# Optimization experiments

Hardware: AMD Instinct MI355X
Metric: run time of the kernel (lower is better)

Reference implementation:

```python
import jax, jax.numpy as jnp
import numpy as np

N_NODES = 100000
N_EDGES = 1600000
NUM_GRAPHS = 1000

def gcn_conv(x, edge_index, W, b, n):
    # PyG GCNConv: out = D^-1/2 (A + I) D^-1/2 (x W) + b
    xw = x @ W                                   # [n, F_out]
    loop = jnp.arange(n, dtype=edge_index.dtype)
    src = jnp.concatenate([edge_index[0], loop])  # sources (messages come from src)
    dst = jnp.concatenate([edge_index[1], loop])  # targets (aggregated into dst)
    deg = jnp.zeros((n,), xw.dtype).at[dst].add(1.0)
    dinv = jnp.where(deg > 0, jax.lax.rsqrt(deg), 0.0)
    norm = dinv[src] * dinv[dst]                  # [E+n]
    msg = xw[src] * norm[:, None]                 # gather + scale
    out = jax.ops.segment_sum(msg, dst, num_segments=n)
    return out + b

def scatter_mean(x, seg, num_segments):
    sums = jax.ops.segment_sum(x, seg, num_segments=num_segments)
    cnt = jax.ops.segment_sum(jnp.ones((x.shape[0],), x.dtype), seg, num_segments=num_segments)
    return sums / jnp.maximum(cnt, 1.0)[:, None]

def setup_inputs() -> dict:
    key = jax.random.key(0)
    ks = jax.random.split(key, 9)
    x = jax.random.normal(ks[0], (N_NODES, 256), dtype=jnp.float32)
    edge_index = jax.random.randint(ks[1], (2, N_EDGES), 0, N_NODES, dtype=jnp.int64 if jax.config.jax_enable_x64 else jnp.int32).astype(jnp.int32)
    batch = jnp.sort(jax.random.randint(ks[2], (N_NODES,), 0, NUM_GRAPHS)).astype(jnp.int32)
    W1 = jax.random.normal(ks[3], (256, 128), dtype=jnp.float32) * 0.05
    b1 = jax.random.normal(ks[4], (128,), dtype=jnp.float32) * 0.05
    W2 = jax.random.normal(ks[5], (128, 64), dtype=jnp.float32) * 0.05
    b2 = jax.random.normal(ks[6], (64,), dtype=jnp.float32) * 0.05
    fc_W = jax.random.normal(ks[7], (64, 4), dtype=jnp.float32) * 0.05
    fc_b = jax.random.normal(ks[8], (4,), dtype=jnp.float32) * 0.05
    return {"x": x, "edge_index": edge_index, "batch": batch, "W1": W1, "b1": b1, "W2": W2, "b2": b2, "fc_W": fc_W, "fc_b": fc_b}

def reference(x, edge_index, batch, W1, b1, W2, b2, fc_W, fc_b):
    n = x.shape[0]
    h = gcn_conv(x, edge_index, W1, b1, n)
    h = jax.nn.relu(h)                 # dropout p=0.0 is identity
    h = gcn_conv(h, edge_index, W2, b2, n)
    g = scatter_mean(h, batch, NUM_GRAPHS)   # [G, out_feats]
    logits = g @ fc_W + fc_b
    return jax.nn.log_softmax(logits, axis=1)
```

## Files before the change

### kernel.cpp

```cpp
#include <hip/hip_runtime.h>
#include <hip/hip_bf16.h>

#define N_NODES 100000
#define N_EDGES 1600000
#define NUM_GRAPHS 1000

#define NODES_PER_BUCKET 256
#define BUCKET_SHIFT 8
#define NBUCKETS 391
#define CAP 5120

#define G1_BLOCKS 1563
#define FUSED_BLOCKS 2345
#define FILL_CHUNK 2052

typedef __attribute__((ext_vector_type(8))) short short8;
typedef __attribute__((ext_vector_type(4))) float f32x4;
typedef __attribute__((ext_vector_type(2))) float f32x2;
typedef unsigned short ushort;

__device__ __forceinline__ ushort f2bf(float f) {
    unsigned int u = __float_as_uint(f);
    u = u + 0x7fffu + ((u >> 16) & 1u);
    return (ushort)(u >> 16);
}
__device__ __forceinline__ float bflo(unsigned int u) { return __uint_as_float(u << 16); }
__device__ __forceinline__ float bfhi(unsigned int u) { return __uint_as_float(u & 0xffff0000u); }

__device__ __forceinline__ unsigned char f2fp8(float f) {
    return (unsigned char)(__builtin_amdgcn_cvt_pk_fp8_f32(f, f, 0, false) & 0xff);
}

__global__ void setup_kernel(int* __restrict__ bcursor,
                             const float* __restrict__ W1, ushort* __restrict__ W1t,
                             const float* __restrict__ W2, ushort* __restrict__ W2t,
                             float* __restrict__ gsum, float* __restrict__ gcnt) {
    int b = blockIdx.x, tid = threadIdx.x;
    if (b < 2) {
        int i = b * 256 + tid;
        if (i < NBUCKETS) bcursor[i] = i * CAP;
    } else if (b < 130) {
        int idx = (b - 2) * 256 + tid;
        int n = idx & 127, k = idx >> 7;
        W1t[n * 256 + k] = f2bf(W1[k * 128 + n]);
    } else if (b < 162) {
        int idx = (b - 130) * 256 + tid;
        int n = idx & 63, k = idx >> 6;
        W2t[n * 128 + k] = f2bf(W2[k * 64 + n]);
    } else {
        int idx = (b - 162) * 256 + tid;
        if (idx < NUM_GRAPHS * 64) gsum[idx] = 0.f;
        else if (idx < NUM_GRAPHS * 64 + NUM_GRAPHS) gcnt[idx - NUM_GRAPHS * 64] = 0.f;
    }
}
#define SETUP_BLOCKS 416

__global__ __launch_bounds__(256) void gemm1_fill_kernel(const float* __restrict__ x,
                                                         const ushort* __restrict__ W1t,
                                                         unsigned char* __restrict__ outb,
                                                         const int* __restrict__ esrc,
                                                         const int* __restrict__ edst,
                                                         int* __restrict__ bcursor,
                                                         int* __restrict__ pairs) {
    __shared__ ushort Ab[64 * 32];
    __shared__ ushort Bb[128 * 32];
    const int b = blockIdx.x;
    const int tid = threadIdx.x;

    if (b % 3 == 2) {
        int* scnt = (int*)Ab;
        int* spos = (int*)Bb;
        const int fid = b / 3;
        const int beg = fid * FILL_CHUNK;
        int end = beg + FILL_CHUNK;
        if (end > N_EDGES) end = N_EDGES;
        if (beg >= end) return;
        for (int i = tid; i < NBUCKETS; i += 256) scnt[i] = 0;
        __syncthreads();
        for (int e = beg + tid * 4; e < end; e += 1024) {
            int4 d4 = *(const int4*)&edst[e];
            atomicAdd(&scnt[d4.x >> BUCKET_SHIFT], 1);
            atomicAdd(&scnt[d4.y >> BUCKET_SHIFT], 1);
            atomicAdd(&scnt[d4.z >> BUCKET_SHIFT], 1);
            atomicAdd(&scnt[d4.w >> BUCKET_SHIFT], 1);
        }
        __syncthreads();
        for (int i = tid; i < NBUCKETS; i += 256) {
            int c = scnt[i];
            spos[i] = c > 0 ? atomicAdd(&bcursor[i], c) : 0;
        }
        __syncthreads();
        for (int e = beg + tid * 4; e < end; e += 1024) {
            int4 d4 = *(const int4*)&edst[e];
            int4 s4 = *(const int4*)&esrc[e];
            int p0 = atomicAdd(&spos[d4.x >> BUCKET_SHIFT], 1);
            pairs[p0] = (s4.x << 8) | (d4.x & 255);
            int p1 = atomicAdd(&spos[d4.y >> BUCKET_SHIFT], 1);
            pairs[p1] = (s4.y << 8) | (d4.y & 255);
            int p2 = atomicAdd(&spos[d4.z >> BUCKET_SHIFT], 1);
            pairs[p2] = (s4.z << 8) | (d4.z & 255);
            int p3 = atomicAdd(&spos[d4.w >> BUCKET_SHIFT], 1);
            pairs[p3] = (s4.w << 8) | (d4.w & 255);
        }
        return;
    }

    const int gid = b - (b + 1) / 3;
    if (gid >= G1_BLOCKS) return;
    const int row0 = gid * 64;
    const int wv = tid >> 6;
    const int l = tid & 63;
    const int lrow = l & 15;
    const int quad = l >> 4;

    const int ar = tid >> 2;
    const int ak = (tid & 3) * 8;
    int grow = row0 + ar;
    if (grow > N_NODES - 1) grow = N_NODES - 1;
    const float* xrow = x + (size_t)grow * 256;
    const int bn = tid >> 1;
    const int bk = (tid & 1) * 16;

    f32x4 acc[8];
#pragma unroll
    for (int t = 0; t < 8; ++t) acc[t] = (f32x4){0.f, 0.f, 0.f, 0.f};

    for (int kc = 0; kc < 8; ++kc) {
        float4 a0 = *(const float4*)&xrow[kc * 32 + ak];
        float4 a1 = *(const float4*)&xrow[kc * 32 + ak + 4];
        const ushort* wt = &W1t[(size_t)bn * 256 + kc * 32 + bk];
        uint4 w0 = *(const uint4*)wt;
        uint4 w1 = *(const uint4*)(wt + 8);

        if (kc > 0) __syncthreads();
        ushort av[8];
        av[0] = f2bf(a0.x); av[1] = f2bf(a0.y); av[2] = f2bf(a0.z); av[3] = f2bf(a0.w);
        av[4] = f2bf(a1.x); av[5] = f2bf(a1.y); av[6] = f2bf(a1.z); av[7] = f2bf(a1.w);
        *(uint4*)&Ab[ar * 32 + ak] = *(uint4*)av;
        *(uint4*)&Bb[bn * 32 + bk] = w0;
        *(uint4*)&Bb[bn * 32 + bk + 8] = w1;
        __syncthreads();

        short8 afrag = *(const short8*)&Ab[(wv * 16 + lrow) * 32 + quad * 8];
#pragma unroll
        for (int t = 0; t < 8; ++t) {
            short8 bfrag = *(const short8*)&Bb[(t * 16 + lrow) * 32 + quad * 8];
            acc[t] = __builtin_amdgcn_mfma_f32_16x16x32_bf16(afrag, bfrag, acc[t], 0, 0, 0);
        }
    }

    const int rbase = row0 + wv * 16 + quad * 4;
#pragma unroll
    for (int t = 0; t < 8; ++t) {
#pragma unroll
        for (int r = 0; r < 4; ++r) {
            int row = rbase + r;
            if (row < N_NODES)
                outb[(size_t)row * 128 + t * 16 + lrow] = f2fp8(acc[t][r]);
        }
    }
}

__global__ __launch_bounds__(256) void csr_fill_local_kernel(const int* __restrict__ pairs,
                                                             const int* __restrict__ bcursor,
                                                             int* __restrict__ csr_src,
                                                             int* __restrict__ row_beg,
                                                             int* __restrict__ row_end,
                                                             float* __restrict__ dinv) {
    __shared__ int plds[CAP];
    __shared__ int hist[256];
    __shared__ int scanv[256];
    __shared__ int cur[256];
    const int b = blockIdx.x;
    const int base = b * CAP;
    const int tid = threadIdx.x;
    const int cnt_b = bcursor[b] - base;

    for (int i = tid; i < cnt_b; i += 256) plds[i] = pairs[base + i];
    hist[tid] = 0;
    __syncthreads();
    for (int i = tid; i < cnt_b; i += 256) atomicAdd(&hist[plds[i] & 255], 1);
    __syncthreads();

    int deg = hist[tid];
    scanv[tid] = deg;
    for (int off = 1; off < 256; off <<= 1) {
        __syncthreads();
        int add = (tid >= off) ? scanv[tid - off] : 0;
        __syncthreads();
        scanv[tid] += add;
    }
    __syncthreads();
    int excl = scanv[tid] - deg;

    int node = b * NODES_PER_BUCKET + tid;
    if (node < N_NODES) {
        int beg = base + excl;
        row_beg[node] = beg;
        row_end[node] = beg + deg;
        dinv[node] = rsqrtf((float)(deg + 1));
    }
    cur[tid] = excl;
    __syncthreads();

    for (int i = tid; i < cnt_b; i += 256) {
        int pr = plds[i];
        int pos = base + atomicAdd(&cur[pr & 255], 1);
        csr_src[pos] = ((unsigned int)pr) >> 8;
    }
}

__global__ __launch_bounds__(256) void agg1_kernel(const unsigned int* __restrict__ xw,
                                                   const int* __restrict__ csr_src,
                                                   const int* __restrict__ row_beg,
                                                   const int* __restrict__ row_end,
                                                   const float* __restrict__ dinv,
                                                   const float* __restrict__ bias,
                                                   ushort* __restrict__ h) {
    const int wave = threadIdx.x >> 6;
    const int lane = threadIdx.x & 63;
    const int h2 = lane >> 5;
    const int c = lane & 31;
    const int node = blockIdx.x * 8 + wave * 2 + h2;

    const int beg = row_beg[node], end = row_end[node];
    const float dvn = rsqrtf((float)(end - beg + 1));

    unsigned int sv = xw[(size_t)node * 32 + c];
    f32x2 slo = __builtin_amdgcn_cvt_pk_f32_fp8(sv, false);
    f32x2 shi = __builtin_amdgcn_cvt_pk_f32_fp8(sv, true);
    float a0 = dvn * slo[0], a1 = dvn * slo[1], a2 = dvn * shi[0], a3 = dvn * shi[1];

    for (int e = beg; e < end; e += 16) {
        int s[16];
        s[0] = csr_src[e];
#pragma unroll
        for (int i = 1; i < 16; ++i)
            s[i] = (e + i < end) ? csr_src[e + i] : s[0];
        unsigned int v[16];
        float ds[16];
#pragma unroll
        for (int i = 0; i < 16; ++i) {
            v[i] = xw[(size_t)s[i] * 32 + c];
            ds[i] = dinv[s[i]];
        }
#pragma unroll
        for (int i = 0; i < 16; ++i) {
            if (i == 0 || e + i < end) {
                f32x2 lo = __builtin_amdgcn_cvt_pk_f32_fp8(v[i], false);
                f32x2 hi = __builtin_amdgcn_cvt_pk_f32_fp8(v[i], true);
                a0 += ds[i] * lo[0]; a1 += ds[i] * lo[1];
                a2 += ds[i] * hi[0]; a3 += ds[i] * hi[1];
            }
        }
    }
    float4 bv = *(const float4*)&bias[c * 4];
    float v0 = a0 * dvn + bv.x, v1 = a1 * dvn + bv.y;
    float v2 = a2 * dvn + bv.z, v3 = a3 * dvn + bv.w;
    ushort4 o;
    o.x = f2bf(v0 > 0.f ? v0 : 0.f);
    o.y = f2bf(v1 > 0.f ? v1 : 0.f);
    o.z = f2bf(v2 > 0.f ? v2 : 0.f);
    o.w = f2bf(v3 > 0.f ? v3 : 0.f);
    *(ushort4*)&h[(size_t)node * 128 + c * 4] = o;
}

__global__ __launch_bounds__(256) void gemm2_kernel(const ushort* __restrict__ h,
                                                    const ushort* __restrict__ W2t,
                                                    unsigned char* __restrict__ outb) {
    __shared__ ushort Ab[64 * 32];
    __shared__ ushort Bb[64 * 32];
    const int tid = threadIdx.x;
    const int row0 = blockIdx.x * 64;
    const int wv = tid >> 6;
    const int l = tid & 63;
    const int lrow = l & 15;
    const int quad = l >> 4;

    const int ar = tid >> 2;
    const int ak = (tid & 3) * 8;
    int grow = row0 + ar;
    if (grow > N_NODES - 1) grow = N_NODES - 1;

    f32x4 acc[4];
#pragma unroll
    for (int t = 0; t < 4; ++t) acc[t] = (f32x4){0.f, 0.f, 0.f, 0.f};

    for (int kc = 0; kc < 4; ++kc) {
        uint4 a = *(const uint4*)&h[(size_t)grow * 128 + kc * 32 + ak];
        uint4 w = *(const uint4*)&W2t[(size_t)ar * 128 + kc * 32 + ak];
        if (kc > 0) __syncthreads();
        *(uint4*)&Ab[ar * 32 + ak] = a;
        *(uint4*)&Bb[ar * 32 + ak] = w;
        __syncthreads();

        short8 afrag = *(const short8*)&Ab[(wv * 16 + lrow) * 32 + quad * 8];
#pragma unroll
        for (int t = 0; t < 4; ++t) {
            short8 bfrag = *(const short8*)&Bb[(t * 16 + lrow) * 32 + quad * 8];
            acc[t] = __builtin_amdgcn_mfma_f32_16x16x32_bf16(afrag, bfrag, acc[t], 0, 0, 0);
        }
    }

    const int rbase = row0 + wv * 16 + quad * 4;
#pragma unroll
    for (int r = 0; r < 4; ++r) {
        int row = rbase + r;
        if (row < N_NODES) {
#pragma unroll
            for (int t = 0; t < 4; ++t)
                outb[(size_t)row * 64 + t * 16 + lrow] = f2fp8(acc[t][r]);
        }
    }
}

__global__ __launch_bounds__(256) void agg2_pool_kernel(const unsigned int* __restrict__ xw,
                                                        const int* __restrict__ csr_src,
                                                        const int* __restrict__ row_beg,
                                                        const int* __restrict__ row_end,
                                                        const float* __restrict__ dinv,
                                                        const float* __restrict__ bias,
                                                        const int* __restrict__ batch,
                                                        float* __restrict__ gsum,
                                                        float* __restrict__ gcnt) {
    __shared__ float part[16][64];
    __shared__ int bsh[16];
    const int wave = threadIdx.x >> 6;
    const int lane = threadIdx.x & 63;
    const int q = lane >> 4;
    const int c = lane & 15;
    const int nl = wave * 4 + q;
    const int node = blockIdx.x * 16 + nl;

    const int beg = row_beg[node], end = row_end[node];
    const float dvn = rsqrtf((float)(end - beg + 1));

    unsigned int sv = xw[(size_t)node * 16 + c];
    f32x2 slo = __builtin_amdgcn_cvt_pk_f32_fp8(sv, false);
    f32x2 shi = __builtin_amdgcn_cvt_pk_f32_fp8(sv, true);
    float a0 = dvn * slo[0], a1 = dvn * slo[1], a2 = dvn * shi[0], a3 = dvn * shi[1];

    for (int e = beg; e < end; e += 16) {
        int s[16];
        s[0] = csr_src[e];
#pragma unroll
        for (int i = 1; i < 16; ++i)
            s[i] = (e + i < end) ? csr_src[e + i] : s[0];
        unsigned int v[16];
        float ds[16];
#pragma unroll
        for (int i = 0; i < 16; ++i) {
            v[i] = xw[(size_t)s[i] * 16 + c];
            ds[i] = dinv[s[i]];
        }
#pragma unroll
        for (int i = 0; i < 16; ++i) {
            if (i == 0 || e + i < end) {
                f32x2 lo = __builtin_amdgcn_cvt_pk_f32_fp8(v[i], false);
                f32x2 hi = __builtin_amdgcn_cvt_pk_f32_fp8(v[i], true);
                a0 += ds[i] * lo[0]; a1 += ds[i] * lo[1];
                a2 += ds[i] * hi[0]; a3 += ds[i] * hi[1];
            }
        }
    }
    float4 bv = *(const float4*)&bias[c * 4];
    float4 val = make_float4(a0 * dvn + bv.x, a1 * dvn + bv.y,
                             a2 * dvn + bv.z, a3 * dvn + bv.w);
    *(float4*)&part[nl][c * 4] = val;
    if (lane == (q << 4)) bsh[nl] = batch[node];
    __syncthreads();

    if (wave == 0) {
        int b0 = bsh[0];
        bool same = true;
#pragma unroll
        for (int i = 1; i < 16; ++i) same = same && (bsh[i] == b0);
        if (same) {
            float s = 0.f;
#pragma unroll
            for (int i = 0; i < 16; ++i) s += part[i][lane];
            atomicAdd(&gsum[b0 * 64 + lane], s);
            if (lane == 0) atomicAdd(&gcnt[b0], 16.0f);
        } else {
#pragma unroll
            for (int i = 0; i < 16; ++i)
                atomicAdd(&gsum[bsh[i] * 64 + lane], part[i][lane]);
            if (lane == 0) {
#pragma unroll
                for (int i = 0; i < 16; ++i) atomicAdd(&gcnt[bsh[i]], 1.0f);
            }
        }
    }
}

__global__ void head_kernel(const float* __restrict__ gsum, const float* __restrict__ gcnt,
                            const float* __restrict__ fcW, const float* __restrict__ fcb,
                            float* __restrict__ out) {
    int g = blockIdx.x * blockDim.x + threadIdx.x;
    if (g >= NUM_GRAPHS) return;
    float c = gcnt[g];
    c = c > 1.f ? c : 1.f;
    float inv = 1.f / c;
    float logits[4];
#pragma unroll
    for (int j = 0; j < 4; ++j) logits[j] = fcb[j];
    for (int k = 0; k < 64; ++k) {
        float m = gsum[g * 64 + k] * inv;
#pragma unroll
        for (int j = 0; j < 4; ++j) logits[j] += m * fcW[k * 4 + j];
    }
    float mx = logits[0];
#pragma unroll
    for (int j = 1; j < 4; ++j) mx = logits[j] > mx ? logits[j] : mx;
    float s = 0.f;
#pragma unroll
    for (int j = 0; j < 4; ++j) s += expf(logits[j] - mx);
    float lse = mx + logf(s);
#pragma unroll
    for (int j = 0; j < 4; ++j) out[g * 4 + j] = logits[j] - lse;
}

extern "C" void kernel_launch(void* const* d_in, const int* in_sizes, int n_in,
                              void* d_out, int out_size, void* d_ws, size_t ws_size,
                              hipStream_t stream) {
    const float* x     = (const float*)d_in[0];
    const int*   ei    = (const int*)d_in[1];
    const int*   batch = (const int*)d_in[2];
    const float* W1    = (const float*)d_in[3];
    const float* b1    = (const float*)d_in[4];
    const float* W2    = (const float*)d_in[5];
    const float* b2    = (const float*)d_in[6];
    const float* fcW   = (const float*)d_in[7];
    const float* fcb   = (const float*)d_in[8];
    float* out = (float*)d_out;

    const int* src = ei;
    const int* dst = ei + N_EDGES;

    size_t o = 0;
    char* wsb = (char*)d_ws;
    auto take = [&](size_t bytes) -> void* {
        void* p = wsb + o;
        o += (bytes + 255) & ~(size_t)255;
        return p;
    };
    float* dinv      = (float*)take((size_t)N_NODES * 4);
    int*   row_beg   = (int*)take((size_t)N_NODES * 4);
    int*   row_end   = (int*)take((size_t)N_NODES * 4);
    int*   bcursor   = (int*)take((size_t)NBUCKETS * 4);
    int*   csr_src   = (int*)take((size_t)NBUCKETS * CAP * 4);
    int*   pairs     = (int*)take((size_t)NBUCKETS * CAP * 4);
    ushort* W1t      = (ushort*)take((size_t)128 * 256 * 2);
    ushort* W2t      = (ushort*)take((size_t)64 * 128 * 2);
    unsigned char* bufA = (unsigned char*)take((size_t)N_NODES * 128);
    ushort* bufB     = (ushort*)take((size_t)N_NODES * 128 * 2);
    float* gsum      = (float*)take((size_t)NUM_GRAPHS * 64 * 4);
    float* gcnt      = (float*)take((size_t)NUM_GRAPHS * 4);
    (void)ws_size;

    const int TB = 256;

    setup_kernel<<<SETUP_BLOCKS, TB, 0, stream>>>(bcursor, W1, W1t, W2, W2t, gsum, gcnt);

    gemm1_fill_kernel<<<FUSED_BLOCKS, TB, 0, stream>>>(x, W1t, bufA, src, dst, bcursor, pairs);

    csr_fill_local_kernel<<<NBUCKETS, TB, 0, stream>>>(pairs, bcursor, csr_src,
                                                       row_beg, row_end, dinv);

    agg1_kernel<<<N_NODES / 8, TB, 0, stream>>>((const unsigned int*)bufA, csr_src,
                                                row_beg, row_end, dinv, b1, bufB);

    gemm2_kernel<<<(N_NODES + 63) / 64, TB, 0, stream>>>(bufB, W2t, bufA);

    agg2_pool_kernel<<<N_NODES / 16, TB, 0, stream>>>((const unsigned int*)bufA, csr_src,
                                                      row_beg, row_end, dinv, b2, batch,
                                                      gsum, gcnt);

    head_kernel<<<(NUM_GRAPHS + TB - 1) / TB, TB, 0, stream>>>(gsum, gcnt, fcW, fcb, out);
}
```

Measured before the change: 314.7 us.

## Drop LDS staging in both GEMMs and register-tile two 64-row halves per block

Both GEMM kernels now load A and B fragments straight from global memory into registers instead of staging them through shared memory, which removes the per-k-chunk __syncthreads. Each wave computes two 16-row tiles, one per 64-row half of a 128-row block, so every B fragment feeds two MFMAs. The fused gemm1/fill kernel changes its interleave from two GEMM blocks per fill block to one-to-one, and gemm2's grid is halved to match. The trade-off is less coalesced global reads for the per-lane fragments and more accumulator registers, which may lower occupancy.

```diff
diff --git a/kernel.cpp b/kernel.cpp
--- a/kernel.cpp
+++ b/kernel.cpp
@@ -10,8 +10,8 @@
 #define NBUCKETS 391
 #define CAP 5120
 
-#define G1_BLOCKS 1563
-#define FUSED_BLOCKS 2345
+#define G1_BLOCKS 782
+#define FUSED_BLOCKS 1563
 #define FILL_CHUNK 2052
 
 typedef __attribute__((ext_vector_type(8))) short short8;
@@ -24,8 +24,6 @@
     u = u + 0x7fffu + ((u >> 16) & 1u);
     return (ushort)(u >> 16);
 }
-__device__ __forceinline__ float bflo(unsigned int u) { return __uint_as_float(u << 16); }
-__device__ __forceinline__ float bfhi(unsigned int u) { return __uint_as_float(u & 0xffff0000u); }
 
 __device__ __forceinline__ unsigned char f2fp8(float f) {
     return (unsigned char)(__builtin_amdgcn_cvt_pk_fp8_f32(f, f, 0, false) & 0xff);
@@ -62,15 +60,13 @@
                                                          const int* __restrict__ edst,
                                                          int* __restrict__ bcursor,
                                                          int* __restrict__ pairs) {
-    __shared__ ushort Ab[64 * 32];
-    __shared__ ushort Bb[128 * 32];
+    __shared__ int scnt[NBUCKETS];
+    __shared__ int spos[NBUCKETS];
     const int b = blockIdx.x;
     const int tid = threadIdx.x;
 
-    if (b % 3 == 2) {
-        int* scnt = (int*)Ab;
-        int* spos = (int*)Bb;
-        const int fid = b / 3;
+    if (b & 1) {
+        const int fid = b >> 1;
         const int beg = fid * FILL_CHUNK;
         int end = beg + FILL_CHUNK;
         if (end > N_EDGES) end = N_EDGES;
@@ -105,58 +101,61 @@
         return;
     }
 
-    const int gid = b - (b + 1) / 3;
-    if (gid >= G1_BLOCKS) return;
-    const int row0 = gid * 64;
+    const int gid = b >> 1;
+    const int row0 = gid * 128;
     const int wv = tid >> 6;
     const int l = tid & 63;
     const int lrow = l & 15;
     const int quad = l >> 4;
 
-    const int ar = tid >> 2;
-    const int ak = (tid & 3) * 8;
-    int grow = row0 + ar;
-    if (grow > N_NODES - 1) grow = N_NODES - 1;
-    const float* xrow = x + (size_t)grow * 256;
-    const int bn = tid >> 1;
-    const int bk = (tid & 1) * 16;
-
-    f32x4 acc[8];
-#pragma unroll
-    for (int t = 0; t < 8; ++t) acc[t] = (f32x4){0.f, 0.f, 0.f, 0.f};
-
+    int r0 = row0 + wv * 16 + lrow;
+    int r1 = r0 + 64;
+    if (r0 > N_NODES - 1) r0 = N_NODES - 1;
+    if (r1 > N_NODES - 1) r1 = N_NODES - 1;
+    const float* xr0 = x + (size_t)r0 * 256 + quad * 8;
+    const float* xr1 = x + (size_t)r1 * 256 + quad * 8;
+    const ushort* wb = W1t + lrow * 256 + quad * 8;
+
+    f32x4 acc[2][8];
+#pragma unroll
+    for (int m = 0; m < 2; ++m)
+#pragma unroll
+        for (int t = 0; t < 8; ++t) acc[m][t] = (f32x4){0.f, 0.f, 0.f, 0.f};
+
+#pragma unroll
     for (int kc = 0; kc < 8; ++kc) {
-        float4 a0 = *(const float4*)&xrow[kc * 32 + ak];
-        float4 a1 = *(const float4*)&xrow[kc * 32 + ak + 4];
-        const ushort* wt = &W1t[(size_t)bn * 256 + kc * 32 + bk];
-        uint4 w0 = *(const uint4*)wt;
-        uint4 w1 = *(const uint4*)(wt + 8);
-
-        if (kc > 0) __syncthreads();
-        ushort av[8];
-        av[0] = f2bf(a0.x); av[1] = f2bf(a0.y); av[2] = f2bf(a0.z); av[3] = f2bf(a0.w);
-        av[4] = f2bf(a1.x); av[5] = f2bf(a1.y); av[6] = f2bf(a1.z); av[7] = f2bf(a1.w);
-        *(uint4*)&Ab[ar * 32 + ak] = *(uint4*)av;
-        *(uint4*)&Bb[bn * 32 + bk] = w0;
-        *(uint4*)&Bb[bn * 32 + bk + 8] = w1;
-        __syncthreads();
-
-        short8 afrag = *(const short8*)&Ab[(wv * 16 + lrow) * 32 + quad * 8];
+        float4 a00 = *(const float4*)(xr0 + kc * 32);
+        float4 a01 = *(const float4*)(xr0 + kc * 32 + 4);
+        float4 a10 = *(const float4*)(xr1 + kc * 32);
+        float4 a11 = *(const float4*)(xr1 + kc * 32 + 4);
+        short8 af0, af1;
+        af0[0] = (short)f2bf(a00.x); af0[1] = (short)f2bf(a00.y);
+        af0[2] = (short)f2bf(a00.z); af0[3] = (short)f2bf(a00.w);
+        af0[4] = (short)f2bf(a01.x); af0[5] = (short)f2bf(a01.y);
+        af0[6] = (short)f2bf(a01.z); af0[7] = (short)f2bf(a01.w);
+        af1[0] = (short)f2bf(a10.x); af1[1] = (short)f2bf(a10.y);
+        af1[2] = (short)f2bf(a10.z); af1[3] = (short)f2bf(a10.w);
+        af1[4] = (short)f2bf(a11.x); af1[5] = (short)f2bf(a11.y);
+        af1[6] = (short)f2bf(a11.z); af1[7] = (short)f2bf(a11.w);
 #pragma unroll
         for (int t = 0; t < 8; ++t) {
-            short8 bfrag = *(const short8*)&Bb[(t * 16 + lrow) * 32 + quad * 8];
-            acc[t] = __builtin_amdgcn_mfma_f32_16x16x32_bf16(afrag, bfrag, acc[t], 0, 0, 0);
-        }
-    }
-
-    const int rbase = row0 + wv * 16 + quad * 4;
-#pragma unroll
-    for (int t = 0; t < 8; ++t) {
-#pragma unroll
-        for (int r = 0; r < 4; ++r) {
-            int row = rbase + r;
-            if (row < N_NODES)
-                outb[(size_t)row * 128 + t * 16 + lrow] = f2fp8(acc[t][r]);
+            short8 bfrag = *(const short8*)(wb + t * 16 * 256 + kc * 32);
+            acc[0][t] = __builtin_amdgcn_mfma_f32_16x16x32_bf16(af0, bfrag, acc[0][t], 0, 0, 0);
+            acc[1][t] = __builtin_amdgcn_mfma_f32_16x16x32_bf16(af1, bfrag, acc[1][t], 0, 0, 0);
+        }
+    }
+
+#pragma unroll
+    for (int m = 0; m < 2; ++m) {
+        const int rbase = row0 + m * 64 + wv * 16 + quad * 4;
+#pragma unroll
+        for (int t = 0; t < 8; ++t) {
+#pragma unroll
+            for (int r = 0; r < 4; ++r) {
+                int row = rbase + r;
+                if (row < N_NODES)
+                    outb[(size_t)row * 128 + t * 16 + lrow] = f2fp8(acc[m][t][r]);
+            }
         }
     }
 }
@@ -268,48 +267,50 @@
 __global__ __launch_bounds__(256) void gemm2_kernel(const ushort* __restrict__ h,
                                                     const ushort* __restrict__ W2t,
                                                     unsigned char* __restrict__ outb) {
-    __shared__ ushort Ab[64 * 32];
-    __shared__ ushort Bb[64 * 32];
     const int tid = threadIdx.x;
-    const int row0 = blockIdx.x * 64;
+    const int row0 = blockIdx.x * 128;
     const int wv = tid >> 6;
     const int l = tid & 63;
     const int lrow = l & 15;
     const int quad = l >> 4;
 
-    const int ar = tid >> 2;
-    const int ak = (tid & 3) * 8;
-    int grow = row0 + ar;
-    if (grow > N_NODES - 1) grow = N_NODES - 1;
-
-    f32x4 acc[4];
-#pragma unroll
-    for (int t = 0; t < 4; ++t) acc[t] = (f32x4){0.f, 0.f, 0.f, 0.f};
-
+    int r0 = row0 + wv * 16 + lrow;
+    int r1 = r0 + 64;
+    if (r0 > N_NODES - 1) r0 = N_NODES - 1;
+    if (r1 > N_NODES - 1) r1 = N_NODES - 1;
+    const ushort* h0 = h + (size_t)r0 * 128 + quad * 8;
+    const ushort* h1 = h + (size_t)r1 * 128 + quad * 8;
+    const ushort* wb = W2t + lrow * 128 + quad * 8;
+
+    f32x4 acc[2][4];
+#pragma unroll
+    for (int m = 0; m < 2; ++m)
+#pragma unroll
+        for (int t = 0; t < 4; ++t) acc[m][t] = (f32x4){0.f, 0.f, 0.f, 0.f};
+
+#pragma unroll
     for (int kc = 0; kc < 4; ++kc) {
-        uint4 a = *(const uint4*)&h[(size_t)grow * 128 + kc * 32 + ak];
-        uint4 w = *(const uint4*)&W2t[(size_t)ar * 128 + kc * 32 + ak];
-        if (kc > 0) __syncthreads();
-        *(uint4*)&Ab[ar * 32 + ak] = a;
-        *(uint4*)&Bb[ar * 32 + ak] = w;
-        __syncthreads();
-
-        short8 afrag = *(const short8*)&Ab[(wv * 16 + lrow) * 32 + quad * 8];
+        short8 af0 = *(const short8*)(h0 + kc * 32);
+        short8 af1 = *(const short8*)(h1 + kc * 32);
 #pragma unroll
         for (int t = 0; t < 4; ++t) {
-            short8 bfrag = *(const short8*)&Bb[(t * 16 + lrow) * 32 + quad * 8];
-            acc[t] = __builtin_amdgcn_mfma_f32_16x16x32_bf16(afrag, bfrag, acc[t], 0, 0, 0);
-        }
-    }
-
-    const int rbase = row0 + wv * 16 + quad * 4;
-#pragma unroll
-    for (int r = 0; r < 4; ++r) {
-        int row = rbase + r;
-        if (row < N_NODES) {
-#pragma unroll
-            for (int t = 0; t < 4; ++t)
-                outb[(size_t)row * 64 + t * 16 + lrow] = f2fp8(acc[t][r]);
+            short8 bfrag = *(const short8*)(wb + t * 16 * 128 + kc * 32);
+            acc[0][t] = __builtin_amdgcn_mfma_f32_16x16x32_bf16(af0, bfrag, acc[0][t], 0, 0, 0);
+            acc[1][t] = __builtin_amdgcn_mfma_f32_16x16x32_bf16(af1, bfrag, acc[1][t], 0, 0, 0);
+        }
+    }
+
+#pragma unroll
+    for (int m = 0; m < 2; ++m) {
+        const int rbase = row0 + m * 64 + wv * 16 + quad * 4;
+#pragma unroll
+        for (int r = 0; r < 4; ++r) {
+            int row = rbase + r;
+            if (row < N_NODES) {
+#pragma unroll
+                for (int t = 0; t < 4; ++t)
+                    outb[(size_t)row * 64 + t * 16 + lrow] = f2fp8(acc[m][t][r]);
+            }
         }
     }
 }
@@ -470,7 +471,7 @@
     agg1_kernel<<<N_NODES / 8, TB, 0, stream>>>((const unsigned int*)bufA, csr_src,
                                                 row_beg, row_end, dinv, b1, bufB);
 
-    gemm2_kernel<<<(N_NODES + 63) / 64, TB, 0, stream>>>(bufB, W2t, bufA);
+    gemm2_kernel<<<(N_NODES + 127) / 128, TB, 0, stream>>>(bufB, W2t, bufA);
 
     agg2_pool_kernel<<<N_NODES / 16, TB, 0, stream>>>((const unsigned int*)bufA, csr_src,
                                                       row_beg, row_end, dinv, b2, batch,
```

After: 348.3 us. +10.7%, slower.
